# Kernel tuning notes

Measured on AMD Instinct MI355X. Metric: run time of the kernel, lower is better.

Reference implementation:

```python
import jax, jax.numpy as jnp
import numpy as np

N = 50000      # nodes
E = 800000     # edges (avg degree 16)
IN = 128       # input feature dim
D = 128        # state_size
B = 10         # bounding_parameter
L = 4          # num_layers
OUT = 40       # out_channels
A = 10.0       # config.a (sigmoid sharpness)


def setup_inputs() -> dict:
    key = jax.random.key(0)
    ks = jax.random.split(key, 6)
    x = jax.random.normal(ks[0], (N, IN), dtype=jnp.float32)
    edge_index = jax.random.randint(ks[1], (2, E), 0, N, dtype=jnp.int64)
    W_in = jax.random.normal(ks[2], (IN, D), dtype=jnp.float32) * 0.05
    b_in = jnp.zeros((D,), jnp.float32)
    W_layers = jax.random.normal(ks[3], (L, D * (B + 1), D), dtype=jnp.float32) * 0.05
    b_layers = jnp.zeros((L, D), jnp.float32)
    W_out = jax.random.normal(ks[4], ((L + 1) * D, OUT), dtype=jnp.float32) * 0.05
    b_out = jnp.zeros((OUT,), jnp.float32)
    return dict(x=x, edge_index=edge_index, W_in=W_in, b_in=b_in,
                W_layers=W_layers, b_layers=b_layers, W_out=W_out, b_out=b_out)


def diff_argmax(x):
    # straight-through argmax: value is one-hot, grad flows through softmax
    y_soft = jax.nn.softmax(x, axis=-1)
    y_hard = jax.nn.one_hot(jnp.argmax(y_soft, axis=-1), x.shape[-1], dtype=x.dtype)
    return jax.lax.stop_gradient(y_hard - y_soft) + y_soft


def reference(x, edge_index, W_in, b_in, W_layers, b_layers, W_out, b_out):
    src, dst = edge_index[0], edge_index[1]
    y_range = jnp.arange(B, dtype=jnp.float32)

    # input layer (LINEAR) + differentiable argmax
    h = diff_argmax(x @ W_in + b_in)          # [N, D]
    xs = [h]
    for l in range(L):
        # scatter-add message aggregation: sum_j x_j over incoming edges
        msg = jax.ops.segment_sum(h[src], dst, num_segments=N)   # [N, D]
        clamped = jnp.clip(msg, 0.0, float(B))
        # bounded expansion: soft thresholds at 0..B-1
        states = jax.nn.sigmoid(A * (jax.nn.elu(clamped[..., None] - y_range) - 0.5))
        states = states.reshape(N, D * B)
        combined = jnp.concatenate([h, states], axis=1)          # [N, D*(B+1)]
        h = diff_argmax(combined @ W_layers[l] + b_layers[l])    # [N, D]
        xs.append(h)

    hcat = jnp.concatenate(xs, axis=1)                           # [N, (L+1)*D]
    logits = jax.nn.log_softmax(hcat @ W_out + b_out, axis=-1)   # [N, OUT]
    return logits
```

## Files before the change

### kernel.cpp

```cpp
#include <hip/hip_runtime.h>
#include <math.h>

#define NN 50000
#define NE 800000
#define DD 128
#define LL 4
#define OUTD 40
#define SCAN_NB ((NN + 255) / 256)
#define NPART 8
#define PART_SZ ((NN + NPART - 1) / NPART)
#define NCHUNK 256
#define CHUNK_E (NE / NCHUNK)
#define NB_T 256
#define NB_IN ((NN + 63) / 64)
#define NB_DEG (NE / 256)

__device__ __forceinline__ float S_func(float t) {
    float z = (t > 0.0f) ? t : expm1f(t);
    float xx = 10.0f * (z - 0.5f);
    return 1.0f / (1.0f + expf(-xx));
}

__global__ __launch_bounds__(256) void front_kernel(
        const float* __restrict__ W_layers, float* __restrict__ T0,
        float* __restrict__ Delta,
        const float* __restrict__ x, const float* __restrict__ W_in,
        const float* __restrict__ b_in, int* __restrict__ idx0,
        const int* __restrict__ dst, unsigned int* __restrict__ deg,
        unsigned int* __restrict__ pos_e) {
    __shared__ float wlds[32][128];
    __shared__ float xls[64][32];
    int t = threadIdx.x;

    if (blockIdx.x < NB_T) {
        int bd = blockIdx.x * 2 + (t >> 7);
        int l = bd >> 7, d = bd & 127;
        int j = t & 127;
        const float* W2 = W_layers + ((size_t)l * 1408 + 128 + (size_t)d * 10) * 128;
        float w[10];
        #pragma unroll
        for (int y = 0; y < 10; ++y) w[y] = W2[(size_t)y * 128 + j];
        float t0 = 0.0f;
        #pragma unroll
        for (int y = 0; y < 10; ++y) t0 += S_func((float)(0 - y)) * w[y];
        T0[(size_t)bd * 128 + j] = t0;
        for (int c = 1; c <= 10; ++c) {
            float tc = 0.0f;
            #pragma unroll
            for (int y = 0; y < 10; ++y) tc += S_func((float)(c - y)) * w[y];
            Delta[((size_t)bd * 10 + (c - 1)) * 128 + j] = tc - t0;
        }
        return;
    }
    if (blockIdx.x >= NB_T + NB_IN) {
        int e = (blockIdx.x - NB_T - NB_IN) * 256 + t;
        if (e < NE) pos_e[e] = atomicAdd(&deg[dst[e]], 1u);
        return;
    }

    int bb = blockIdx.x - NB_T;
    int cg = t & 15;
    int ng = t >> 4;
    int n0 = bb * 64;
    float acc[4][8];
    #pragma unroll
    for (int i = 0; i < 4; ++i)
        #pragma unroll
        for (int r = 0; r < 8; ++r) acc[i][r] = 0.0f;

    for (int kc = 0; kc < 4; ++kc) {
        __syncthreads();
        #pragma unroll
        for (int p = 0; p < 4; ++p) {
            int f = t + p * 256;
            int kr = f >> 5, c4 = f & 31;
            *(float4*)&wlds[kr][c4 * 4] =
                *(const float4*)&W_in[(size_t)(kc * 32 + kr) * 128 + c4 * 4];
        }
        #pragma unroll
        for (int p = 0; p < 2; ++p) {
            int f = t + p * 256;
            int node = f >> 3, k4 = f & 7;
            int gn = n0 + node;
            if (gn > NN - 1) gn = NN - 1;
            *(float4*)&xls[node][k4 * 4] =
                *(const float4*)&x[(size_t)gn * 128 + kc * 32 + k4 * 4];
        }
        __syncthreads();
        #pragma unroll
        for (int kk4 = 0; kk4 < 8; ++kk4) {
            float4 xv[4];
            #pragma unroll
            for (int i = 0; i < 4; ++i)
                xv[i] = *(const float4*)&xls[ng * 4 + i][kk4 * 4];
            #pragma unroll
            for (int q = 0; q < 4; ++q) {
                int k = kk4 * 4 + q;
                float4 w1 = *(const float4*)&wlds[k][cg * 4];
                float4 w2 = *(const float4*)&wlds[k][64 + cg * 4];
                #pragma unroll
                for (int i = 0; i < 4; ++i) {
                    float xvv = (q == 0) ? xv[i].x : (q == 1) ? xv[i].y
                              : (q == 2) ? xv[i].z : xv[i].w;
                    acc[i][0] = fmaf(xvv, w1.x, acc[i][0]);
                    acc[i][1] = fmaf(xvv, w1.y, acc[i][1]);
                    acc[i][2] = fmaf(xvv, w1.z, acc[i][2]);
                    acc[i][3] = fmaf(xvv, w1.w, acc[i][3]);
                    acc[i][4] = fmaf(xvv, w2.x, acc[i][4]);
                    acc[i][5] = fmaf(xvv, w2.y, acc[i][5]);
                    acc[i][6] = fmaf(xvv, w2.z, acc[i][6]);
                    acc[i][7] = fmaf(xvv, w2.w, acc[i][7]);
                }
            }
        }
    }
    float4 b1 = *(const float4*)&b_in[cg * 4];
    float4 b2 = *(const float4*)&b_in[64 + cg * 4];
    #pragma unroll
    for (int i = 0; i < 4; ++i) {
        float v0 = acc[i][0] + b1.x, v1 = acc[i][1] + b1.y;
        float v2 = acc[i][2] + b1.z, v3 = acc[i][3] + b1.w;
        float v4 = acc[i][4] + b2.x, v5 = acc[i][5] + b2.y;
        float v6 = acc[i][6] + b2.z, v7 = acc[i][7] + b2.w;
        float bv = v0; int bi = cg * 4;
        if (v1 > bv) { bv = v1; bi = cg * 4 + 1; }
        if (v2 > bv) { bv = v2; bi = cg * 4 + 2; }
        if (v3 > bv) { bv = v3; bi = cg * 4 + 3; }
        if (v4 > bv) { bv = v4; bi = 64 + cg * 4; }
        if (v5 > bv) { bv = v5; bi = 64 + cg * 4 + 1; }
        if (v6 > bv) { bv = v6; bi = 64 + cg * 4 + 2; }
        if (v7 > bv) { bv = v7; bi = 64 + cg * 4 + 3; }
        #pragma unroll
        for (int o = 8; o >= 1; o >>= 1) {
            float ov = __shfl_xor(bv, o);
            int oi = __shfl_xor(bi, o);
            if (ov > bv || (ov == bv && oi < bi)) { bv = ov; bi = oi; }
        }
        int n = n0 + ng * 4 + i;
        if (cg == 0 && n < NN) idx0[n] = bi;
    }
}

__global__ void build_Base(const float* __restrict__ T0, float* __restrict__ Base) {
    int l = blockIdx.x, j = threadIdx.x;
    float s = 0.0f;
    for (int d = 0; d < 128; ++d) s += T0[((size_t)l * 128 + d) * 128 + j];
    Base[l * 128 + j] = s;
}

__global__ __launch_bounds__(256) void partial_kernel(const unsigned int* __restrict__ deg,
        unsigned int* __restrict__ blocksum) {
    __shared__ unsigned int wsum[4];
    int t = threadIdx.x;
    int i = blockIdx.x * 256 + t;
    int w = t >> 6, lane = t & 63;
    unsigned int v = (i < NN) ? deg[i] : 0u;
    #pragma unroll
    for (int o = 32; o >= 1; o >>= 1) v += __shfl_xor(v, o);
    if (lane == 0) wsum[w] = v;
    __syncthreads();
    if (t == 0) blocksum[blockIdx.x] = wsum[0] + wsum[1] + wsum[2] + wsum[3];
}

__global__ __launch_bounds__(256) void final_scan(const unsigned int* __restrict__ deg,
        const unsigned int* __restrict__ blocksum, unsigned int* __restrict__ rowptr) {
    __shared__ unsigned int wsum[4];
    __shared__ unsigned int presh;
    int t = threadIdx.x;
    int w = t >> 6, lane = t & 63;
    unsigned int pv = (t < blockIdx.x) ? blocksum[t] : 0u;
    #pragma unroll
    for (int o = 32; o >= 1; o >>= 1) pv += __shfl_xor(pv, o);
    if (lane == 0) wsum[w] = pv;
    __syncthreads();
    if (t == 0) presh = wsum[0] + wsum[1] + wsum[2] + wsum[3];
    __syncthreads();
    unsigned int blockpre = presh;
    __syncthreads();
    int i = blockIdx.x * 256 + t;
    unsigned int v = (i < NN) ? deg[i] : 0u;
    unsigned int s = v;
    #pragma unroll
    for (int o = 1; o < 64; o <<= 1) {
        unsigned int u = __shfl_up(s, o, 64);
        if (lane >= o) s += u;
    }
    if (lane == 63) wsum[w] = s;
    __syncthreads();
    unsigned int pre = blockpre;
    for (int k = 0; k < w; ++k) pre += wsum[k];
    if (i < NN) rowptr[i + 1] = pre + s;
    if (i == 0) rowptr[0] = 0u;
}

__global__ __launch_bounds__(256) void scatter_kernel(const int* __restrict__ src,
        const int* __restrict__ dst, const unsigned int* __restrict__ rowptr,
        const unsigned int* __restrict__ pos_e, int* __restrict__ col) {
    int part = blockIdx.x & (NPART - 1);
    int chunk = blockIdx.x >> 3;
    int lo = part * PART_SZ, hi = lo + PART_SZ;
    int e0 = chunk * CHUNK_E;
    int e1 = e0 + CHUNK_E;
    for (int e = e0 + threadIdx.x; e < e1; e += 256) {
        int d = dst[e];
        int s = src[e];
        unsigned int p = pos_e[e];
        if (d >= lo && d < hi) col[rowptr[d] + p] = s;
    }
}

__global__ __launch_bounds__(256) void layer_kernel(
        const unsigned int* __restrict__ rowptr, const int* __restrict__ col,
        const float* __restrict__ Wl, const float* __restrict__ bl,
        const float* __restrict__ Delta_l, const float* __restrict__ Base_l,
        const int* __restrict__ idx_in, int* __restrict__ idx_out) {
    __shared__ unsigned int cnt[8][128];
    __shared__ int list[8][128];
    int w = threadIdx.x >> 6;
    int lane = threadIdx.x & 63;
    int h = lane >> 5, l = lane & 31;
    int nidx = w * 2 + h;
    int n = blockIdx.x * 8 + nidx;
    unsigned int rs = rowptr[n], re = rowptr[n + 1];
    int hidx = idx_in[n];
    float4 wv = *(const float4*)((const char*)Wl + (size_t)hidx * 512 + l * 16);
    float4 bs = *(const float4*)((const char*)Base_l + l * 16);
    float4 bb = *(const float4*)((const char*)bl + l * 16);
    cnt[nidx][l]      = 0u;
    cnt[nidx][l + 32] = 0u;
    cnt[nidx][l + 64] = 0u;
    cnt[nidx][l + 96] = 0u;
    for (unsigned int e = rs + l; e < re; e += 32u) {
        int s = col[e];
        atomicAdd(&cnt[nidx][idx_in[s]], 1u);
    }
    unsigned int c0 = cnt[nidx][4 * l];
    unsigned int c1 = cnt[nidx][4 * l + 1];
    unsigned int c2 = cnt[nidx][4 * l + 2];
    unsigned int c3 = cnt[nidx][4 * l + 3];
    int f0 = c0 != 0u, f1 = c1 != 0u, f2 = c2 != 0u, f3 = c3 != 0u;
    int nb = f0 + f1 + f2 + f3;
    int incl = nb;
    #pragma unroll
    for (int o = 1; o < 32; o <<= 1) {
        int u = __shfl_up(incl, o, 32);
        if (l >= o) incl += u;
    }
    int pos = incl - nb;
    int total = __shfl(incl, 31, 32);
    if (f0) { unsigned int cc = c0 > 10u ? 10u : c0;
              list[nidx][pos++] = (int)(((4 * l + 0) * 10 + (int)cc - 1) * 512); }
    if (f1) { unsigned int cc = c1 > 10u ? 10u : c1;
              list[nidx][pos++] = (int)(((4 * l + 1) * 10 + (int)cc - 1) * 512); }
    if (f2) { unsigned int cc = c2 > 10u ? 10u : c2;
              list[nidx][pos++] = (int)(((4 * l + 2) * 10 + (int)cc - 1) * 512); }
    if (f3) { unsigned int cc = c3 > 10u ? 10u : c3;
              list[nidx][pos++] = (int)(((4 * l + 3) * 10 + (int)cc - 1) * 512); }
    float4 acc;
    acc.x = wv.x + bs.x;
    acc.y = wv.y + bs.y;
    acc.z = wv.z + bs.z;
    acc.w = wv.w + bs.w;
    const char* Db = (const char*)Delta_l + l * 16;
    int i = 0;
    for (; i + 8 <= total; i += 8) {
        int o0 = list[nidx][i];
        int o1 = list[nidx][i + 1];
        int o2 = list[nidx][i + 2];
        int o3 = list[nidx][i + 3];
        int o4 = list[nidx][i + 4];
        int o5 = list[nidx][i + 5];
        int o6 = list[nidx][i + 6];
        int o7 = list[nidx][i + 7];
        float4 d0 = *(const float4*)(Db + o0);
        float4 d1 = *(const float4*)(Db + o1);
        float4 d2 = *(const float4*)(Db + o2);
        float4 d3 = *(const float4*)(Db + o3);
        float4 d4 = *(const float4*)(Db + o4);
        float4 d5 = *(const float4*)(Db + o5);
        float4 d6 = *(const float4*)(Db + o6);
        float4 d7 = *(const float4*)(Db + o7);
        acc.x += d0.x; acc.y += d0.y; acc.z += d0.z; acc.w += d0.w;
        acc.x += d1.x; acc.y += d1.y; acc.z += d1.z; acc.w += d1.w;
        acc.x += d2.x; acc.y += d2.y; acc.z += d2.z; acc.w += d2.w;
        acc.x += d3.x; acc.y += d3.y; acc.z += d3.z; acc.w += d3.w;
        acc.x += d4.x; acc.y += d4.y; acc.z += d4.z; acc.w += d4.w;
        acc.x += d5.x; acc.y += d5.y; acc.z += d5.z; acc.w += d5.w;
        acc.x += d6.x; acc.y += d6.y; acc.z += d6.z; acc.w += d6.w;
        acc.x += d7.x; acc.y += d7.y; acc.z += d7.z; acc.w += d7.w;
    }
    for (; i + 4 <= total; i += 4) {
        int o0 = list[nidx][i];
        int o1 = list[nidx][i + 1];
        int o2 = list[nidx][i + 2];
        int o3 = list[nidx][i + 3];
        float4 d0 = *(const float4*)(Db + o0);
        float4 d1 = *(const float4*)(Db + o1);
        float4 d2 = *(const float4*)(Db + o2);
        float4 d3 = *(const float4*)(Db + o3);
        acc.x += d0.x; acc.y += d0.y; acc.z += d0.z; acc.w += d0.w;
        acc.x += d1.x; acc.y += d1.y; acc.z += d1.z; acc.w += d1.w;
        acc.x += d2.x; acc.y += d2.y; acc.z += d2.z; acc.w += d2.w;
        acc.x += d3.x; acc.y += d3.y; acc.z += d3.z; acc.w += d3.w;
    }
    for (; i < total; ++i) {
        float4 dv = *(const float4*)(Db + list[nidx][i]);
        acc.x += dv.x; acc.y += dv.y; acc.z += dv.z; acc.w += dv.w;
    }
    acc.x += bb.x; acc.y += bb.y; acc.z += bb.z; acc.w += bb.w;
    float bv = acc.x; int bi = 4 * l;
    if (acc.y > bv) { bv = acc.y; bi = 4 * l + 1; }
    if (acc.z > bv) { bv = acc.z; bi = 4 * l + 2; }
    if (acc.w > bv) { bv = acc.w; bi = 4 * l + 3; }
    #pragma unroll
    for (int o = 16; o >= 1; o >>= 1) {
        float ov = __shfl_xor(bv, o);
        int oi = __shfl_xor(bi, o);
        if (ov > bv || (ov == bv && oi < bi)) { bv = ov; bi = oi; }
    }
    if (l == 0) idx_out[n] = bi;
}

__global__ __launch_bounds__(256) void output_kernel(const int* __restrict__ idx,
        const float* __restrict__ W_out, const float* __restrict__ b_out,
        float* __restrict__ out) {
    int w = threadIdx.x >> 6;
    int o = threadIdx.x & 63;
    int n = blockIdx.x * 4 + w;
    if (n >= NN) return;
    float v;
    if (o < OUTD) {
        float a = 0.0f;
        #pragma unroll
        for (int l = 0; l < 5; ++l) {
            int id = idx[(size_t)l * NN + n];
            a += W_out[((size_t)(l * 128 + id)) * OUTD + o];
        }
        v = a + b_out[o];
    } else {
        v = -INFINITY;
    }
    float mx = v;
    #pragma unroll
    for (int s = 32; s >= 1; s >>= 1) mx = fmaxf(mx, __shfl_xor(mx, s));
    float e = (o < OUTD) ? expf(v - mx) : 0.0f;
    float se = e;
    #pragma unroll
    for (int s = 32; s >= 1; s >>= 1) se += __shfl_xor(se, s);
    if (o < OUTD) out[(size_t)n * OUTD + o] = v - mx - logf(se);
}

extern "C" void kernel_launch(void* const* d_in, const int* in_sizes, int n_in,
                              void* d_out, int out_size, void* d_ws, size_t ws_size,
                              hipStream_t stream) {
    const float* x        = (const float*)d_in[0];
    const int*   edge     = (const int*)d_in[1];
    const float* W_in     = (const float*)d_in[2];
    const float* b_in     = (const float*)d_in[3];
    const float* W_layers = (const float*)d_in[4];
    const float* b_layers = (const float*)d_in[5];
    const float* W_out    = (const float*)d_in[6];
    const float* b_out    = (const float*)d_in[7];
    float* out = (float*)d_out;

    char* ws = (char*)d_ws;
    size_t off = 0;
    float* Delta = (float*)(ws + off); off += (size_t)LL * 128 * 10 * 128 * 4;
    float* T0    = (float*)(ws + off); off += (size_t)LL * 128 * 128 * 4;
    float* Base  = (float*)(ws + off); off += (size_t)LL * 128 * 4;
    int*   idx   = (int*)(ws + off);   off += (size_t)(LL + 1) * NN * 4;
    unsigned int* deg    = (unsigned int*)(ws + off); off += (size_t)NN * 4;
    unsigned int* rowptr = (unsigned int*)(ws + off); off += (size_t)(NN + 8) * 4;
    unsigned int* blocksum = (unsigned int*)(ws + off); off += 256 * 4;
    unsigned int* pos_e  = (unsigned int*)(ws + off); off += (size_t)NE * 4;
    int*   col   = (int*)(ws + off);   off += (size_t)NE * 4;

    const int* srcp = edge;
    const int* dstp = edge + NE;

    hipMemsetAsync(deg, 0, (size_t)NN * 4, stream);
    hipLaunchKernelGGL(front_kernel, dim3(NB_T + NB_IN + NB_DEG), dim3(256), 0, stream,
                       W_layers, T0, Delta, x, W_in, b_in, idx, dstp, deg, pos_e);
    hipLaunchKernelGGL(build_Base, dim3(LL), dim3(128), 0, stream, T0, Base);
    hipLaunchKernelGGL(partial_kernel, dim3(SCAN_NB), dim3(256), 0, stream, deg, blocksum);
    hipLaunchKernelGGL(final_scan, dim3(SCAN_NB), dim3(256), 0, stream, deg, blocksum, rowptr);
    hipLaunchKernelGGL(scatter_kernel, dim3(NPART * NCHUNK), dim3(256), 0, stream,
                       srcp, dstp, rowptr, pos_e, col);

    for (int l = 0; l < LL; ++l) {
        hipLaunchKernelGGL(layer_kernel, dim3(NN / 8), dim3(256), 0, stream,
                           rowptr, col,
                           W_layers + (size_t)l * 1408 * 128,
                           b_layers + (size_t)l * 128,
                           Delta + (size_t)l * 128 * 10 * 128,
                           Base + (size_t)l * 128,
                           idx + (size_t)l * NN,
                           idx + (size_t)(l + 1) * NN);
    }
    hipLaunchKernelGGL(output_kernel, dim3((NN + 3) / 4), dim3(256), 0, stream,
                       idx, W_out, b_out, out);
}
```

Before: 198.1 us.

## Replace per-edge position array with partitioned degree counting and scatter cursors

Degree counting now uses the same destination-partitioned chunking as the scatter pass, and the per-edge pos_e array is dropped. The scatter kernel takes slots from a per-node cursor with atomicAdd instead of reading precomputed positions. This cuts a full edge-sized write and read and localizes atomics by node partition, at the cost of a second atomic pass in scatter. Column order within each row becomes nondeterministic. The xls shared array is also padded to cut bank conflicts.

```diff
diff --git a/kernel.cpp b/kernel.cpp
--- a/kernel.cpp
+++ b/kernel.cpp
@@ -13,7 +13,7 @@
 #define CHUNK_E (NE / NCHUNK)
 #define NB_T 256
 #define NB_IN ((NN + 63) / 64)
-#define NB_DEG (NE / 256)
+#define NB_DEG (NPART * NCHUNK)
 
 __device__ __forceinline__ float S_func(float t) {
     float z = (t > 0.0f) ? t : expm1f(t);
@@ -26,10 +26,9 @@
         float* __restrict__ Delta,
         const float* __restrict__ x, const float* __restrict__ W_in,
         const float* __restrict__ b_in, int* __restrict__ idx0,
-        const int* __restrict__ dst, unsigned int* __restrict__ deg,
-        unsigned int* __restrict__ pos_e) {
+        const int* __restrict__ dst, unsigned int* __restrict__ deg) {
     __shared__ float wlds[32][128];
-    __shared__ float xls[64][32];
+    __shared__ float xls[64][36];
     int t = threadIdx.x;
 
     if (blockIdx.x < NB_T) {
@@ -53,8 +52,15 @@
         return;
     }
     if (blockIdx.x >= NB_T + NB_IN) {
-        int e = (blockIdx.x - NB_T - NB_IN) * 256 + t;
-        if (e < NE) pos_e[e] = atomicAdd(&deg[dst[e]], 1u);
+        int bb = blockIdx.x - NB_T - NB_IN;
+        int part = bb & (NPART - 1);
+        int chunk = bb >> 3;
+        int lo = part * PART_SZ, hi = lo + PART_SZ;
+        int e0 = chunk * CHUNK_E, e1 = e0 + CHUNK_E;
+        for (int e = e0 + t; e < e1; e += 256) {
+            int d = dst[e];
+            if (d >= lo && d < hi) atomicAdd(&deg[d], 1u);
+        }
         return;
     }
 
@@ -195,7 +201,7 @@
 
 __global__ __launch_bounds__(256) void scatter_kernel(const int* __restrict__ src,
         const int* __restrict__ dst, const unsigned int* __restrict__ rowptr,
-        const unsigned int* __restrict__ pos_e, int* __restrict__ col) {
+        unsigned int* __restrict__ cursor, int* __restrict__ col) {
     int part = blockIdx.x & (NPART - 1);
     int chunk = blockIdx.x >> 3;
     int lo = part * PART_SZ, hi = lo + PART_SZ;
@@ -204,8 +210,10 @@
     for (int e = e0 + threadIdx.x; e < e1; e += 256) {
         int d = dst[e];
         int s = src[e];
-        unsigned int p = pos_e[e];
-        if (d >= lo && d < hi) col[rowptr[d] + p] = s;
+        if (d >= lo && d < hi) {
+            unsigned int pos = atomicAdd(&cursor[d], 1u);
+            col[rowptr[d] + pos] = s;
+        }
     }
 }
 
@@ -370,22 +378,22 @@
     float* Base  = (float*)(ws + off); off += (size_t)LL * 128 * 4;
     int*   idx   = (int*)(ws + off);   off += (size_t)(LL + 1) * NN * 4;
     unsigned int* deg    = (unsigned int*)(ws + off); off += (size_t)NN * 4;
+    unsigned int* cursor = (unsigned int*)(ws + off); off += (size_t)NN * 4;
     unsigned int* rowptr = (unsigned int*)(ws + off); off += (size_t)(NN + 8) * 4;
     unsigned int* blocksum = (unsigned int*)(ws + off); off += 256 * 4;
-    unsigned int* pos_e  = (unsigned int*)(ws + off); off += (size_t)NE * 4;
     int*   col   = (int*)(ws + off);   off += (size_t)NE * 4;
 
     const int* srcp = edge;
     const int* dstp = edge + NE;
 
-    hipMemsetAsync(deg, 0, (size_t)NN * 4, stream);
+    hipMemsetAsync(deg, 0, (size_t)2 * NN * 4, stream);
     hipLaunchKernelGGL(front_kernel, dim3(NB_T + NB_IN + NB_DEG), dim3(256), 0, stream,
-                       W_layers, T0, Delta, x, W_in, b_in, idx, dstp, deg, pos_e);
+                       W_layers, T0, Delta, x, W_in, b_in, idx, dstp, deg);
     hipLaunchKernelGGL(build_Base, dim3(LL), dim3(128), 0, stream, T0, Base);
     hipLaunchKernelGGL(partial_kernel, dim3(SCAN_NB), dim3(256), 0, stream, deg, blocksum);
     hipLaunchKernelGGL(final_scan, dim3(SCAN_NB), dim3(256), 0, stream, deg, blocksum, rowptr);
     hipLaunchKernelGGL(scatter_kernel, dim3(NPART * NCHUNK), dim3(256), 0, stream,
-                       srcp, dstp, rowptr, pos_e, col);
+                       srcp, dstp, rowptr, cursor, col);
 
     for (int l = 0; l < LL; ++l) {
         hipLaunchKernelGGL(layer_kernel, dim3(NN / 8), dim3(256), 0, stream,
```

Result: slower. 226.7 us (+14.5%).
